# Optimization experiments

Hardware: AMD Instinct MI355X
Metric: run time of the kernel (lower is better)

## Reference

```python
import jax, jax.numpy as jnp
from jax import lax
import numpy as np
import math

D = 96   # d_model
H = 4    # num_heads (d_k = d_v = D per head, per the source)
K = 7    # depthwise kernel size
L = 4    # num conv layers


def _pos_encoding(seq_len, d):
    # Faithful to the source's (nonstandard) exponents: sin uses 2*i/d, cos uses 2*(i+1)/d
    pos = np.arange(seq_len, dtype=np.float32)[:, None]
    i = np.arange(0, d, 2, dtype=np.float32)
    pe = np.zeros((seq_len, d), dtype=np.float32)
    pe[:, 0::2] = np.sin(pos / 10000.0 ** (2.0 * i / d))
    pe[:, 1::2] = np.cos(pos / 10000.0 ** (2.0 * (i + 1.0) / d))
    return jnp.asarray(pe)


def _layernorm(x, g, b, eps=1e-5):
    m = jnp.mean(x, axis=-1, keepdims=True)
    v = jnp.mean((x - m) ** 2, axis=-1, keepdims=True)
    return (x - m) / jnp.sqrt(v + eps) * g + b


def setup_inputs() -> dict:
    key = jax.random.key(0)
    ks = jax.random.split(key, 10)
    B, S = 128, 384

    def xavier(k, shape, fan_in, fan_out):
        bound = math.sqrt(6.0 / (fan_in + fan_out))
        return jax.random.uniform(k, shape, jnp.float32, -bound, bound)

    return {
        "input": jax.random.normal(ks[0], (B, S, D), jnp.float32),
        "mask": jnp.zeros((B, S), dtype=bool),
        "conv_dw": jax.random.normal(ks[1], (L, D, 1, K), jnp.float32) * 0.05,
        "conv_dw_b": jnp.zeros((L, D), jnp.float32),
        "conv_pw": jax.random.normal(ks[2], (L, D, D, 1), jnp.float32) * 0.05,
        "conv_pw_b": jnp.zeros((L, D), jnp.float32),
        "WQ": xavier(ks[3], (H, D, D), D, D),
        "WK": xavier(ks[4], (H, D, D), D, D),
        "WV": xavier(ks[5], (H, D, D), D, D),
        "WO": xavier(ks[6], (H * D, D), H * D, D),
        "ffn_w1": jax.random.normal(ks[7], (D, D // 2), jnp.float32) * 0.1,
        "ffn_b1": jnp.zeros((D // 2,), jnp.float32),
        "ffn_w2": jax.random.normal(ks[8], (D // 2, D), jnp.float32) * 0.1,
        "ffn_b2": jnp.zeros((D,), jnp.float32),
        "ln_g": jnp.ones((L + 2, D), jnp.float32),
        "ln_b": jnp.zeros((L + 2, D), jnp.float32),
    }


def reference(input, mask, conv_dw, conv_dw_b, conv_pw, conv_pw_b,
              WQ, WK, WV, WO, ffn_w1, ffn_b1, ffn_w2, ffn_b2, ln_g, ln_b):
    B, S, _ = input.shape
    dn = ("NCH", "OIH", "NCH")

    # positional encoding (eval mode: all dropout is identity)
    x = input * jnp.float32(math.sqrt(D)) + _pos_encoding(S, D)[None]

    # conv blocks: LN -> depthwise conv -> pointwise conv -> relu -> residual
    for i in range(L):
        h = _layernorm(x, ln_g[i], ln_b[i])
        h = jnp.transpose(h, (0, 2, 1))  # [B, C, S]
        h = lax.conv_general_dilated(h, conv_dw[i], (1,), "SAME",
                                     feature_group_count=D, dimension_numbers=dn)
        h = h + conv_dw_b[i][None, :, None]
        h = lax.conv_general_dilated(h, conv_pw[i], (1,), "SAME", dimension_numbers=dn)
        h = jax.nn.relu(h + conv_pw_b[i][None, :, None])
        x = x + jnp.transpose(h, (0, 2, 1))

    # multi-head attention with per-head full-width projections (d_k = D)
    h = _layernorm(x, ln_g[L], ln_b[L])
    Q = jnp.einsum("bsd,hde->hbse", h, WQ)
    Kh = jnp.einsum("bsd,hde->hbse", h, WK)
    V = jnp.einsum("bsd,hde->hbse", h, WV)
    # source divides scores by temperature = 1/sqrt(d_k) => multiply by sqrt(D)
    scores = jnp.einsum("hbqe,hbke->hbqk", Q, Kh) * jnp.float32(math.sqrt(D))
    # mask is viewed [B, S, 1]: masks query rows, broadcast over keys
    scores = jnp.where(mask[None, :, :, None], -jnp.inf, scores)
    attn = jax.nn.softmax(scores, axis=-1)
    ctx = jnp.einsum("hbqk,hbke->hbqe", attn, V)
    cat = jnp.transpose(ctx, (1, 2, 0, 3)).reshape(B, S, H * D)
    x = x + cat @ WO

    # feed-forward: Linear -> sigmoid -> Linear, residual
    h2 = _layernorm(x, ln_g[L + 1], ln_b[L + 1])
    ff = jax.nn.sigmoid(h2 @ ffn_w1 + ffn_b1) @ ffn_w2 + ffn_b2
    return x + ff
```

## Files before the change

### kernel.cpp

```cpp
#include <hip/hip_runtime.h>
#include <math.h>


constexpr int B = 128;
constexpr int S = 384;
constexpr int D = 96;
constexpr int H = 4;
constexpr int KW = 7;
constexpr int L = 4;
constexpr int ROWS = B * S;
constexpr long long NTOT = (long long)ROWS * D;
constexpr float SQRTD = 9.797958971132712f;

typedef _Float16 f16x8 __attribute__((ext_vector_type(8)));
typedef float f32x4 __attribute__((ext_vector_type(4)));
typedef unsigned short us;
typedef unsigned short us8 __attribute__((ext_vector_type(8)));

__device__ __forceinline__ us f2h(float f) {
    _Float16 h = (_Float16)f;
    return __builtin_bit_cast(us, h);
}
__device__ __forceinline__ f16x8 ldh(const us* p) {
    return *reinterpret_cast<const f16x8*>(p);
}

__global__ void pe_kernel(float* __restrict__ pe) {
    int idx = blockIdx.x * 256 + threadIdx.x;
    if (idx >= S * D) return;
    int s = idx / D, c = idx - s * D;
    int j = c >> 1;
    float expo = (c & 1) ? (4.0f * j + 2.0f) / 96.0f : (4.0f * j) / 96.0f;
    float freq = expf(-expo * logf(10000.0f));
    float ang = (float)s * freq;
    pe[idx] = (c & 1) ? cosf(ang) : sinf(ang);
}

__global__ void prep_w(const float* __restrict__ WQ, const float* __restrict__ WK,
                       const float* __restrict__ cpw, const float* __restrict__ w1,
                       const float* __restrict__ w2,
                       us* __restrict__ wqS, us* __restrict__ wkS, us* __restrict__ pwS,
                       us* __restrict__ w1S, us* __restrict__ w2S) {
    int idx = blockIdx.x * 256 + threadIdx.x;
    if (idx >= H * D * D) return;
    int h = idx / (D * D), rem = idx - h * (D * D);
    int d = rem / D, e = rem - d * D;
    int n = e >> 4, lmod = e & 15, kk = d >> 5, ldiv = (d >> 3) & 3, j = d & 7;
    size_t fi = (size_t)(((n * 3 + kk) * 64 + ldiv * 16 + lmod) * 8 + j);
    wqS[(size_t)h * D * D + fi] = f2h(WQ[idx] * SQRTD);
    wkS[(size_t)h * D * D + fi] = f2h(WK[idx]);
    {
        int l = idx / (D * D);
        int o = rem / D, c = rem - o * D;
        int no = o >> 4, lo = o & 15, kc = c >> 5, lc = (c >> 3) & 3, jc = c & 7;
        pwS[(size_t)l * D * D + (size_t)(((no * 3 + kc) * 64 + lc * 16 + lo) * 8 + jc)] =
            f2h(cpw[idx]);
    }
    if (idx < 48 * 96) {
        int m = idx / 96, c = idx - m * 96;
        int nm = m >> 4, lm = m & 15, kc = c >> 5, lc = (c >> 3) & 3, jc = c & 7;
        w1S[((nm * 3 + kc) * 64 + lc * 16 + lm) * 8 + jc] = f2h(w1[c * 48 + m]);
    }
    if (idx < 96 * 64) {
        int o = idx / 64, mk = idx - o * 64;
        int no = o >> 4, lo = o & 15, km = mk >> 5, lm2 = (mk >> 3) & 3, jm = mk & 7;
        w2S[((no * 2 + km) * 64 + lm2 * 16 + lo) * 8 + jm] =
            (mk < 48) ? f2h(w2[mk * 96 + o]) : (us)0;
    }
}

__global__ void prep_wvo(const float* __restrict__ WV, const float* __restrict__ WO,
                         us* __restrict__ wvoS) {
    int blk = blockIdx.x;
    int h = blk / 6, ot = blk - h * 6;
    int tid = threadIdx.x;
    const float* wv = WV + (size_t)h * D * D;
    const float* wo = WO + (size_t)h * D * D;
    for (int i = tid; i < 16 * 96; i += 256) {
        int lmod = i / 96, d = i - (i / 96) * 96;
        int o = ot * 16 + lmod;
        float acc = 0.f;
        for (int e = 0; e < 96; e++) acc += wv[d * 96 + e] * wo[e * 96 + o];
        int kk = d >> 5, ldiv = (d >> 3) & 3, j = d & 7;
        wvoS[(size_t)h * D * D + (size_t)(((ot * 3 + kk) * 64 + ldiv * 16 + lmod) * 8 + j)] =
            f2h(acc);
    }
}

__global__ void conv0f(const float* __restrict__ in, const float* __restrict__ pe,
                       const float* __restrict__ g0, const float* __restrict__ b0,
                       float* __restrict__ xout, us* __restrict__ lnout,
                       const float* __restrict__ dwW, const float* __restrict__ dwB,
                       const us* __restrict__ pwW, const float* __restrict__ pwb,
                       const float* __restrict__ gnext, const float* __restrict__ bnext) {
    __shared__ us lnb_s[70 * 104];
    __shared__ us dwb_s[64 * 104];
    __shared__ float lw[96 * 8];
    int tid = threadIdx.x;
    int wave = tid >> 6, lane = tid & 63;
    int r0 = blockIdx.x * 64;
    int b = r0 / S, s0 = r0 % S;

    for (int i = tid; i < 96 * KW; i += 256) lw[(i / KW) * 8 + (i % KW)] = dwW[i];

    for (int i = wave; i < 70; i += 4) {
        int s = s0 - 3 + i;
        bool valid = (unsigned)s < (unsigned)S;
        float v0 = 0.f, v1 = 0.f;
        if (valid) {
            size_t ro = ((size_t)b * S + s) * 96;
            v0 = in[ro + lane] * SQRTD + pe[s * 96 + lane];
            v1 = (lane < 32) ? in[ro + 64 + lane] * SQRTD + pe[s * 96 + 64 + lane] : 0.f;
        }
        float sm = v0 + v1, q = v0 * v0 + v1 * v1;
        for (int off = 32; off > 0; off >>= 1) {
            sm += __shfl_xor(sm, off);
            q += __shfl_xor(q, off);
        }
        float mean = sm * (1.0f / D);
        float var = q * (1.0f / D) - mean * mean;
        float rstd = rsqrtf(var + 1e-5f);
        lnb_s[i * 104 + lane] = f2h(valid ? (v0 - mean) * rstd * g0[lane] + b0[lane] : 0.f);
        if (lane < 32)
            lnb_s[i * 104 + 64 + lane] =
                f2h(valid ? (v1 - mean) * rstd * g0[lane + 64] + b0[lane + 64] : 0.f);
    }
    __syncthreads();

    for (int u = tid; u < 768; u += 256) {
        int j = u / 12, c0 = (u - (u / 12) * 12) * 8;
        float acc[8];
        #pragma unroll
        for (int j2 = 0; j2 < 8; j2++) acc[j2] = dwB[c0 + j2];
        #pragma unroll
        for (int k = 0; k < KW; k++) {
            f16x8 v = ldh(&lnb_s[(j + k) * 104 + c0]);
            #pragma unroll
            for (int j2 = 0; j2 < 8; j2++) acc[j2] += (float)v[j2] * lw[(c0 + j2) * 8 + k];
        }
        us8 o;
        #pragma unroll
        for (int j2 = 0; j2 < 8; j2++) o[j2] = f2h(acc[j2]);
        *reinterpret_cast<us8*>(&dwb_s[j * 104 + c0]) = o;
    }
    __syncthreads();

    int lmod = lane & 15, ldiv = lane >> 4, m0 = wave * 16;
    f32x4 acc[6] = {};
    #pragma unroll
    for (int kk = 0; kk < 3; kk++) {
        f16x8 af = ldh(&dwb_s[(m0 + lmod) * 104 + kk * 32 + ldiv * 8]);
        #pragma unroll
        for (int n = 0; n < 6; n++) {
            f16x8 bf = ldh(pwW + (size_t)((n * 3 + kk) * 64) * 8 + lane * 8);
            acc[n] = __builtin_amdgcn_mfma_f32_16x16x32_f16(af, bf, acc[n], 0, 0, 0);
        }
    }

    float gv[6], bv2[6], pb[6];
    #pragma unroll
    for (int n = 0; n < 6; n++) {
        int o = n * 16 + lmod;
        gv[n] = gnext[o];
        bv2[n] = bnext[o];
        pb[n] = pwb[o];
    }
    #pragma unroll
    for (int n = 0; n < 6; n++) {
        int o = n * 16 + lmod;
        #pragma unroll
        for (int r = 0; r < 4; r++) {
            int sr = m0 + ldiv * 4 + r;
            size_t row = (size_t)r0 + sr;
            float base = in[row * 96 + o] * SQRTD + pe[(s0 + sr) * 96 + o];
            acc[n][r] = base + fmaxf(acc[n][r] + pb[n], 0.f);
        }
    }
    #pragma unroll
    for (int r = 0; r < 4; r++) {
        float sm = 0.f, qq = 0.f;
        #pragma unroll
        for (int n = 0; n < 6; n++) {
            sm += acc[n][r];
            qq += acc[n][r] * acc[n][r];
        }
        #pragma unroll
        for (int st = 1; st <= 8; st <<= 1) {
            sm += __shfl_xor(sm, st);
            qq += __shfl_xor(qq, st);
        }
        float mean = sm * (1.0f / D);
        float var = qq * (1.0f / D) - mean * mean;
        float rstd = rsqrtf(var + 1e-5f);
        size_t row = (size_t)r0 + m0 + ldiv * 4 + r;
        #pragma unroll
        for (int n = 0; n < 6; n++) {
            int o = n * 16 + lmod;
            xout[row * 96 + o] = acc[n][r];
            lnout[row * 96 + o] = f2h((acc[n][r] - mean) * rstd * gv[n] + bv2[n]);
        }
    }
}

__global__ void conv2(const float* __restrict__ xin, const us* __restrict__ lnin,
                      float* __restrict__ xout, us* __restrict__ lnout,
                      const float* __restrict__ dwW, const float* __restrict__ dwB,
                      const us* __restrict__ pwW, const float* __restrict__ pwb,
                      const float* __restrict__ gnext, const float* __restrict__ bnext) {
    __shared__ us dwb_s[64 * 104];
    __shared__ float lw[96 * 8];
    int tid = threadIdx.x;
    int wave = tid >> 6, lane = tid & 63;
    int r0 = blockIdx.x * 64;
    int b = r0 / S, s0 = r0 % S;

    for (int i = tid; i < 96 * KW; i += 256) lw[(i / KW) * 8 + (i % KW)] = dwW[i];
    __syncthreads();

    for (int u = tid; u < 768; u += 256) {
        int j = u / 12, c0 = (u - (u / 12) * 12) * 8;
        float acc[8];
        #pragma unroll
        for (int j2 = 0; j2 < 8; j2++) acc[j2] = dwB[c0 + j2];
        #pragma unroll
        for (int k = 0; k < KW; k++) {
            int ss = s0 + j + k - 3;
            if ((unsigned)ss < (unsigned)S) {
                f16x8 v = ldh(lnin + ((size_t)b * S + ss) * 96 + c0);
                #pragma unroll
                for (int j2 = 0; j2 < 8; j2++) acc[j2] += (float)v[j2] * lw[(c0 + j2) * 8 + k];
            }
        }
        us8 o;
        #pragma unroll
        for (int j2 = 0; j2 < 8; j2++) o[j2] = f2h(acc[j2]);
        *reinterpret_cast<us8*>(&dwb_s[j * 104 + c0]) = o;
    }
    __syncthreads();

    int lmod = lane & 15, ldiv = lane >> 4, m0 = wave * 16;
    f32x4 acc[6] = {};
    #pragma unroll
    for (int kk = 0; kk < 3; kk++) {
        f16x8 af = ldh(&dwb_s[(m0 + lmod) * 104 + kk * 32 + ldiv * 8]);
        #pragma unroll
        for (int n = 0; n < 6; n++) {
            f16x8 bf = ldh(pwW + (size_t)((n * 3 + kk) * 64) * 8 + lane * 8);
            acc[n] = __builtin_amdgcn_mfma_f32_16x16x32_f16(af, bf, acc[n], 0, 0, 0);
        }
    }

    float gv[6], bv2[6], pb[6];
    #pragma unroll
    for (int n = 0; n < 6; n++) {
        int o = n * 16 + lmod;
        gv[n] = gnext[o];
        bv2[n] = bnext[o];
        pb[n] = pwb[o];
    }
    #pragma unroll
    for (int n = 0; n < 6; n++) {
        #pragma unroll
        for (int r = 0; r < 4; r++) {
            size_t row = (size_t)r0 + m0 + ldiv * 4 + r;
            acc[n][r] = xin[row * 96 + n * 16 + lmod] + fmaxf(acc[n][r] + pb[n], 0.f);
        }
    }
    #pragma unroll
    for (int r = 0; r < 4; r++) {
        float sm = 0.f, qq = 0.f;
        #pragma unroll
        for (int n = 0; n < 6; n++) {
            sm += acc[n][r];
            qq += acc[n][r] * acc[n][r];
        }
        #pragma unroll
        for (int st = 1; st <= 8; st <<= 1) {
            sm += __shfl_xor(sm, st);
            qq += __shfl_xor(qq, st);
        }
        float mean = sm * (1.0f / D);
        float var = qq * (1.0f / D) - mean * mean;
        float rstd = rsqrtf(var + 1e-5f);
        size_t row = (size_t)r0 + m0 + ldiv * 4 + r;
        #pragma unroll
        for (int n = 0; n < 6; n++) {
            int o = n * 16 + lmod;
            xout[row * 96 + o] = acc[n][r];
            lnout[row * 96 + o] = f2h((acc[n][r] - mean) * rstd * gv[n] + bv2[n]);
        }
    }
}

__global__ void conv3p(const float* __restrict__ xin, const us* __restrict__ lnin,
                       float* __restrict__ xout, us* __restrict__ lnout,
                       const float* __restrict__ dwW, const float* __restrict__ dwB,
                       const us* __restrict__ pwW, const float* __restrict__ pwb,
                       const float* __restrict__ gnext, const float* __restrict__ bnext,
                       const us* __restrict__ wkS, const us* __restrict__ wvoS,
                       us* __restrict__ Kall, us* __restrict__ Vall) {
    __shared__ float lw[96 * 8];
    __shared__ us stg[96 * 72];
    __shared__ us lnstg[64 * 104];
    int tid = threadIdx.x;
    int wave = tid >> 6, lane = tid & 63;
    int lmod = lane & 15, ldiv = lane >> 4, m0 = wave * 16;
    int r0 = blockIdx.x * 64;
    int b = r0 / S, s0 = r0 % S;

    for (int i = tid; i < 96 * KW; i += 256) lw[(i / KW) * 8 + (i % KW)] = dwW[i];
    __syncthreads();

    for (int u = tid; u < 768; u += 256) {
        int j = u / 12, c0 = (u - (u / 12) * 12) * 8;
        float acc[8];
        #pragma unroll
        for (int j2 = 0; j2 < 8; j2++) acc[j2] = dwB[c0 + j2];
        #pragma unroll
        for (int k = 0; k < KW; k++) {
            int ss = s0 + j + k - 3;
            if ((unsigned)ss < (unsigned)S) {
                f16x8 v = ldh(lnin + ((size_t)b * S + ss) * 96 + c0);
                #pragma unroll
                for (int j2 = 0; j2 < 8; j2++) acc[j2] += (float)v[j2] * lw[(c0 + j2) * 8 + k];
            }
        }
        us8 o;
        #pragma unroll
        for (int j2 = 0; j2 < 8; j2++) o[j2] = f2h(acc[j2]);
        *reinterpret_cast<us8*>(&stg[j * 104 + c0]) = o;
    }
    __syncthreads();

    f32x4 acc[6] = {};
    #pragma unroll
    for (int kk = 0; kk < 3; kk++) {
        f16x8 af = ldh(&stg[(m0 + lmod) * 104 + kk * 32 + ldiv * 8]);
        #pragma unroll
        for (int n = 0; n < 6; n++) {
            f16x8 bf = ldh(pwW + (size_t)((n * 3 + kk) * 64) * 8 + lane * 8);
            acc[n] = __builtin_amdgcn_mfma_f32_16x16x32_f16(af, bf, acc[n], 0, 0, 0);
        }
    }

    float gv[6], bv2[6], pb[6];
    #pragma unroll
    for (int n = 0; n < 6; n++) {
        int o = n * 16 + lmod;
        gv[n] = gnext[o];
        bv2[n] = bnext[o];
        pb[n] = pwb[o];
    }
    #pragma unroll
    for (int n = 0; n < 6; n++) {
        #pragma unroll
        for (int r = 0; r < 4; r++) {
            size_t row = (size_t)r0 + m0 + ldiv * 4 + r;
            acc[n][r] = xin[row * 96 + n * 16 + lmod] + fmaxf(acc[n][r] + pb[n], 0.f);
        }
    }
    #pragma unroll
    for (int r = 0; r < 4; r++) {
        float sm = 0.f, qq = 0.f;
        #pragma unroll
        for (int n = 0; n < 6; n++) {
            sm += acc[n][r];
            qq += acc[n][r] * acc[n][r];
        }
        #pragma unroll
        for (int st = 1; st <= 8; st <<= 1) {
            sm += __shfl_xor(sm, st);
            qq += __shfl_xor(qq, st);
        }
        float mean = sm * (1.0f / D);
        float var = qq * (1.0f / D) - mean * mean;
        float rstd = rsqrtf(var + 1e-5f);
        size_t row = (size_t)r0 + m0 + ldiv * 4 + r;
        #pragma unroll
        for (int n = 0; n < 6; n++) {
            int o = n * 16 + lmod;
            xout[row * 96 + o] = acc[n][r];
            us hv = f2h((acc[n][r] - mean) * rstd * gv[n] + bv2[n]);
            lnout[row * 96 + o] = hv;
            lnstg[(m0 + ldiv * 4 + r) * 104 + o] = hv;
        }
    }
    __syncthreads();

    f16x8 af[3];
    #pragma unroll
    for (int kk = 0; kk < 3; kk++)
        af[kk] = ldh(&lnstg[(m0 + lmod) * 104 + kk * 32 + ldiv * 8]);

    for (int hd = 0; hd < H; hd++) {
        f32x4 ka[6] = {};
        #pragma unroll
        for (int kk = 0; kk < 3; kk++)
            #pragma unroll
            for (int n = 0; n < 6; n++) {
                f16x8 bf = ldh(wkS + (size_t)hd * D * D + (size_t)((n * 3 + kk) * 64) * 8 + lane * 8);
                ka[n] = __builtin_amdgcn_mfma_f32_16x16x32_f16(af[kk], bf, ka[n], 0, 0, 0);
            }
        __syncthreads();
        us* kT = stg + wave * 1664;
        #pragma unroll
        for (int n = 0; n < 6; n++)
            #pragma unroll
            for (int r = 0; r < 4; r++)
                kT[(ldiv * 4 + r) * 104 + n * 16 + lmod] = f2h(ka[n][r]);
        int t0 = (r0 % S) / 16 + wave;
        us* dst = Kall + (size_t)hd * NTOT + ((size_t)(b * 24 + t0) * 3) * 512;
        #pragma unroll
        for (int kk = 0; kk < 3; kk++) {
            us8 v = *reinterpret_cast<const us8*>(&kT[lmod * 104 + kk * 32 + ldiv * 8]);
            *reinterpret_cast<us8*>(dst + kk * 512 + lane * 8) = v;
        }
        f32x4 va[6] = {};
        #pragma unroll
        for (int kk = 0; kk < 3; kk++)
            #pragma unroll
            for (int n = 0; n < 6; n++) {
                f16x8 bf =
                    ldh(wvoS + (size_t)hd * D * D + (size_t)((n * 3 + kk) * 64) * 8 + lane * 8);
                va[n] = __builtin_amdgcn_mfma_f32_16x16x32_f16(af[kk], bf, va[n], 0, 0, 0);
            }
        __syncthreads();
        #pragma unroll
        for (int n = 0; n < 6; n++)
            #pragma unroll
            for (int r = 0; r < 4; r++)
                stg[(n * 16 + lmod) * 72 + m0 + ldiv * 4 + r] = f2h(va[n][r]);
        __syncthreads();
        int cblk = (r0 % S) / 64;
        us* dsth = Vall + (size_t)hd * NTOT;
        #pragma unroll
        for (int n = 0; n < 6; n++)
            #pragma unroll
            for (int kk = 0; kk < 2; kk++) {
                us8 v =
                    *reinterpret_cast<const us8*>(&stg[(n * 16 + lmod) * 72 + kk * 32 + ldiv * 8]);
                *reinterpret_cast<us8*>(
                    dsth + ((size_t)((b * 6 + cblk) * 6 + n) * 2 + kk) * 512 + lane * 8) = v;
            }
    }
}

__global__ __launch_bounds__(256, 2) void attn_g(const us* __restrict__ h16,
                                                 const us* __restrict__ wqS,
                                                 const us* __restrict__ Kall,
                                                 const us* __restrict__ Vall,
                                                 us* __restrict__ xpart) {
    __shared__ us Kb[2][6144];
    __shared__ us Vb[2][6144];
    __shared__ us Pq[4][3328];
    int tid = threadIdx.x, wave = tid >> 6, lane = tid & 63;
    int lmod = lane & 15, ldiv = lane >> 4;
    int p = blockIdx.x;
    int gl = (p & 7) * 192 + (p >> 3);
    int qt = gl % 3;
    int bh = gl / 3;
    int b = bh >> 2, hd = bh & 3;
    size_t rowbase = (size_t)b * S + qt * 128 + wave * 32;

    const us* Kh = Kall + (size_t)hd * NTOT + (size_t)b * 24 * 1536;
    const us* Vh = Vall + (size_t)hd * NTOT + (size_t)b * 36 * 1024;
    us* P = Pq[wave];

    us8 kst[3];
    #pragma unroll
    for (int j = 0; j < 3; j++)
        kst[j] = *reinterpret_cast<const us8*>(Kh + (size_t)(j * 256 + tid) * 8);

    f32x4 qa0[6] = {}, qa1[6] = {};
    #pragma unroll
    for (int kk = 0; kk < 3; kk++) {
        f16x8 a0 = ldh(h16 + (rowbase + lmod) * 96 + kk * 32 + ldiv * 8);
        f16x8 a1 = ldh(h16 + (rowbase + 16 + lmod) * 96 + kk * 32 + ldiv * 8);
        #pragma unroll
        for (int n = 0; n < 6; n++) {
            f16x8 bf = ldh(wqS + (size_t)hd * D * D + (size_t)((n * 3 + kk) * 64) * 8 + lane * 8);
            qa0[n] = __builtin_amdgcn_mfma_f32_16x16x32_f16(a0, bf, qa0[n], 0, 0, 0);
            qa1[n] = __builtin_amdgcn_mfma_f32_16x16x32_f16(a1, bf, qa1[n], 0, 0, 0);
        }
    }
    #pragma unroll
    for (int n = 0; n < 6; n++)
        #pragma unroll
        for (int r = 0; r < 4; r++) {
            P[(ldiv * 4 + r) * 104 + n * 16 + lmod] = f2h(qa0[n][r]);
            P[(16 + ldiv * 4 + r) * 104 + n * 16 + lmod] = f2h(qa1[n][r]);
        }
    f16x8 aq0[3], aq1[3];
    #pragma unroll
    for (int kk = 0; kk < 3; kk++) {
        aq0[kk] = ldh(&P[lmod * 104 + kk * 32 + ldiv * 8]);
        aq1[kk] = ldh(&P[(16 + lmod) * 104 + kk * 32 + ldiv * 8]);
    }
    #pragma unroll
    for (int j = 0; j < 3; j++)
        *reinterpret_cast<us8*>(&Kb[0][(j * 256 + tid) * 8]) = kst[j];
    __syncthreads();

    f32x4 mx0 = {-1e30f, -1e30f, -1e30f, -1e30f}, mx1 = mx0;
    for (int c = 0; c < 6; c++) {
        int cur = c & 1, nxt = cur ^ 1;
        us8 kn[3], vn[3];
        bool last = (c == 5);
        if (!last) {
            #pragma unroll
            for (int j = 0; j < 3; j++)
                kn[j] = *reinterpret_cast<const us8*>(Kh + (size_t)(c + 1) * 6144 +
                                                      (size_t)(j * 256 + tid) * 8);
        } else {
            #pragma unroll
            for (int j = 0; j < 3; j++) {
                kn[j] = *reinterpret_cast<const us8*>(Kh + (size_t)(j * 256 + tid) * 8);
                vn[j] = *reinterpret_cast<const us8*>(Vh + (size_t)(j * 256 + tid) * 8);
            }
        }
        __builtin_amdgcn_s_setprio(1);
        f32x4 s0[4] = {}, s1[4] = {};
        #pragma unroll
        for (int nt = 0; nt < 4; nt++)
            #pragma unroll
            for (int kk = 0; kk < 3; kk++) {
                f16x8 bf = ldh(&Kb[cur][(nt * 3 + kk) * 512 + lane * 8]);
                s0[nt] = __builtin_amdgcn_mfma_f32_16x16x32_f16(aq0[kk], bf, s0[nt], 0, 0, 0);
                s1[nt] = __builtin_amdgcn_mfma_f32_16x16x32_f16(aq1[kk], bf, s1[nt], 0, 0, 0);
            }
        __builtin_amdgcn_s_setprio(0);
        #pragma unroll
        for (int nt = 0; nt < 4; nt++)
            #pragma unroll
            for (int r = 0; r < 4; r++) {
                mx0[r] = fmaxf(mx0[r], s0[nt][r]);
                mx1[r] = fmaxf(mx1[r], s1[nt][r]);
            }
        int wb = last ? 0 : nxt;
        #pragma unroll
        for (int j = 0; j < 3; j++)
            *reinterpret_cast<us8*>(&Kb[wb][(j * 256 + tid) * 8]) = kn[j];
        if (last) {
            #pragma unroll
            for (int j = 0; j < 3; j++)
                *reinterpret_cast<us8*>(&Vb[0][(j * 256 + tid) * 8]) = vn[j];
        }
        __syncthreads();
    }
    #pragma unroll
    for (int st = 1; st <= 8; st <<= 1)
        #pragma unroll
        for (int r = 0; r < 4; r++) {
            mx0[r] = fmaxf(mx0[r], __shfl_xor(mx0[r], st));
            mx1[r] = fmaxf(mx1[r], __shfl_xor(mx1[r], st));
        }

    f32x4 oacc0[6] = {}, oacc1[6] = {};
    f32x4 l0v = {}, l1v = {};
    for (int c = 0; c < 6; c++) {
        int cur = c & 1, nxt = cur ^ 1;
        us8 kn[3], vn[3];
        if (c < 5) {
            #pragma unroll
            for (int j = 0; j < 3; j++) {
                kn[j] = *reinterpret_cast<const us8*>(Kh + (size_t)(c + 1) * 6144 +
                                                      (size_t)(j * 256 + tid) * 8);
                vn[j] = *reinterpret_cast<const us8*>(Vh + (size_t)(c + 1) * 6144 +
                                                      (size_t)(j * 256 + tid) * 8);
            }
        }
        __builtin_amdgcn_s_setprio(1);
        f32x4 s0[4] = {}, s1[4] = {};
        #pragma unroll
        for (int nt = 0; nt < 4; nt++)
            #pragma unroll
            for (int kk = 0; kk < 3; kk++) {
                f16x8 bf = ldh(&Kb[cur][(nt * 3 + kk) * 512 + lane * 8]);
                s0[nt] = __builtin_amdgcn_mfma_f32_16x16x32_f16(aq0[kk], bf, s0[nt], 0, 0, 0);
                s1[nt] = __builtin_amdgcn_mfma_f32_16x16x32_f16(aq1[kk], bf, s1[nt], 0, 0, 0);
            }
        __builtin_amdgcn_s_setprio(0);
        #pragma unroll
        for (int nt = 0; nt < 4; nt++)
            #pragma unroll
            for (int r = 0; r < 4; r++) {
                float p0 = __expf(s0[nt][r] - mx0[r]);
                float p1 = __expf(s1[nt][r] - mx1[r]);
                l0v[r] += p0;
                l1v[r] += p1;
                P[(ldiv * 4 + r) * 72 + nt * 16 + lmod] = f2h(p0);
                P[(16 + ldiv * 4 + r) * 72 + nt * 16 + lmod] = f2h(p1);
            }
        __builtin_amdgcn_s_setprio(1);
        #pragma unroll
        for (int kk = 0; kk < 2; kk++) {
            f16x8 pf0 = ldh(&P[lmod * 72 + kk * 32 + ldiv * 8]);
            f16x8 pf1 = ldh(&P[(16 + lmod) * 72 + kk * 32 + ldiv * 8]);
            #pragma unroll
            for (int n = 0; n < 6; n++) {
                f16x8 bf = ldh(&Vb[cur][(n * 2 + kk) * 512 + lane * 8]);
                oacc0[n] = __builtin_amdgcn_mfma_f32_16x16x32_f16(pf0, bf, oacc0[n], 0, 0, 0);
                oacc1[n] = __builtin_amdgcn_mfma_f32_16x16x32_f16(pf1, bf, oacc1[n], 0, 0, 0);
            }
        }
        __builtin_amdgcn_s_setprio(0);
        if (c < 5) {
            #pragma unroll
            for (int j = 0; j < 3; j++) {
                *reinterpret_cast<us8*>(&Kb[nxt][(j * 256 + tid) * 8]) = kn[j];
                *reinterpret_cast<us8*>(&Vb[nxt][(j * 256 + tid) * 8]) = vn[j];
            }
            __syncthreads();
        }
    }
    #pragma unroll
    for (int st = 1; st <= 8; st <<= 1)
        #pragma unroll
        for (int r = 0; r < 4; r++) {
            l0v[r] += __shfl_xor(l0v[r], st);
            l1v[r] += __shfl_xor(l1v[r], st);
        }

    us* xp = xpart + (size_t)hd * NTOT;
    #pragma unroll
    for (int r = 0; r < 4; r++) {
        float inv0 = 1.f / l0v[r];
        float inv1 = 1.f / l1v[r];
        #pragma unroll
        for (int n = 0; n < 6; n++) {
            xp[(rowbase + ldiv * 4 + r) * 96 + n * 16 + lmod] = f2h(oacc0[n][r] * inv0);
            xp[(rowbase + 16 + ldiv * 4 + r) * 96 + n * 16 + lmod] = f2h(oacc1[n][r] * inv1);
        }
    }
}

__global__ void ffn_ln(const float* __restrict__ x, const us* __restrict__ xpart,
                       const float* __restrict__ gln, const float* __restrict__ bln,
                       const us* __restrict__ w1S, const float* __restrict__ b1,
                       const us* __restrict__ w2S, const float* __restrict__ b2,
                       float* __restrict__ out) {
    __shared__ float xf[64 * 96];
    __shared__ us lnb[64 * 104];
    __shared__ us mid[64 * 72];
    int tid = threadIdx.x, wave = tid >> 6, lane = tid & 63;
    int lmod = lane & 15, ldiv = lane >> 4, m0 = wave * 16;
    int row0 = blockIdx.x * 64;

    for (int i = wave; i < 64; i += 4) {
        size_t ro = (size_t)(row0 + i) * 96;
        float v0 = x[ro + lane];
        float v1 = (lane < 32) ? x[ro + 64 + lane] : 0.f;
        #pragma unroll
        for (int h = 0; h < H; h++) {
            const us* xp = xpart + (size_t)h * NTOT + ro;
            v0 += (float)__builtin_bit_cast(_Float16, xp[lane]);
            if (lane < 32) v1 += (float)__builtin_bit_cast(_Float16, xp[64 + lane]);
        }
        xf[i * 96 + lane] = v0;
        if (lane < 32) xf[i * 96 + 64 + lane] = v1;
        float sm = v0 + v1, q = v0 * v0 + v1 * v1;
        for (int off = 32; off > 0; off >>= 1) {
            sm += __shfl_xor(sm, off);
            q += __shfl_xor(q, off);
        }
        float mean = sm * (1.0f / D);
        float var = q * (1.0f / D) - mean * mean;
        float rstd = rsqrtf(var + 1e-5f);
        lnb[i * 104 + lane] = f2h((v0 - mean) * rstd * gln[lane] + bln[lane]);
        if (lane < 32)
            lnb[i * 104 + 64 + lane] = f2h((v1 - mean) * rstd * gln[lane + 64] + bln[lane + 64]);
    }
    __syncthreads();

    f32x4 a3[3] = {};
    #pragma unroll
    for (int kk = 0; kk < 3; kk++) {
        f16x8 af = ldh(&lnb[(m0 + lmod) * 104 + kk * 32 + ldiv * 8]);
        #pragma unroll
        for (int n = 0; n < 3; n++) {
            f16x8 bf = ldh(w1S + (size_t)((n * 3 + kk) * 64) * 8 + lane * 8);
            a3[n] = __builtin_amdgcn_mfma_f32_16x16x32_f16(af, bf, a3[n], 0, 0, 0);
        }
    }
    #pragma unroll
    for (int n = 0; n < 3; n++) {
        float bv = b1[n * 16 + lmod];
        #pragma unroll
        for (int r = 0; r < 4; r++) {
            float v = a3[n][r] + bv;
            mid[(m0 + ldiv * 4 + r) * 72 + n * 16 + lmod] = f2h(1.f / (1.f + __expf(-v)));
        }
    }
    #pragma unroll
    for (int r = 0; r < 4; r++) mid[(m0 + ldiv * 4 + r) * 72 + 48 + lmod] = 0;
    __syncthreads();

    f32x4 a6[6] = {};
    #pragma unroll
    for (int kk = 0; kk < 2; kk++) {
        f16x8 af = ldh(&mid[(m0 + lmod) * 72 + kk * 32 + ldiv * 8]);
        #pragma unroll
        for (int n = 0; n < 6; n++) {
            f16x8 bf = ldh(w2S + (size_t)((n * 2 + kk) * 64) * 8 + lane * 8);
            a6[n] = __builtin_amdgcn_mfma_f32_16x16x32_f16(af, bf, a6[n], 0, 0, 0);
        }
    }
    #pragma unroll
    for (int n = 0; n < 6; n++) {
        int o = n * 16 + lmod;
        float bv = b2[o];
        #pragma unroll
        for (int r = 0; r < 4; r++) {
            int sr = m0 + ldiv * 4 + r;
            out[(size_t)(row0 + sr) * 96 + o] = xf[sr * 96 + o] + a6[n][r] + bv;
        }
    }
}

extern "C" void kernel_launch(void* const* d_in, const int* in_sizes, int n_in,
                              void* d_out, int out_size, void* d_ws, size_t ws_size,
                              hipStream_t stream) {
    const float* in   = (const float*)d_in[0];
    const float* cdw  = (const float*)d_in[2];
    const float* cdwb = (const float*)d_in[3];
    const float* cpw  = (const float*)d_in[4];
    const float* cpwb = (const float*)d_in[5];
    const float* WQ   = (const float*)d_in[6];
    const float* WK   = (const float*)d_in[7];
    const float* WV   = (const float*)d_in[8];
    const float* WO   = (const float*)d_in[9];
    const float* w1   = (const float*)d_in[10];
    const float* b1   = (const float*)d_in[11];
    const float* w2   = (const float*)d_in[12];
    const float* b2   = (const float*)d_in[13];
    const float* lng  = (const float*)d_in[14];
    const float* lnb  = (const float*)d_in[15];
    float* out = (float*)d_out;
    float* ws = (float*)d_ws;

    float* xA  = ws;
    float* xB  = xA + NTOT;
    float* pe  = xB + NTOT;
    us* lnA    = (us*)(pe + S * D);
    us* lnB    = lnA + NTOT;
    us* Kall   = lnB + NTOT;
    us* Vall   = Kall + (size_t)H * NTOT;
    us* xpart  = Vall + (size_t)H * NTOT;
    us* wqS    = xpart + (size_t)H * NTOT;
    us* wkS    = wqS + H * D * D;
    us* wvoS   = wkS + H * D * D;
    us* pwS    = wvoS + H * D * D;
    us* w1S    = pwS + L * D * D;
    us* w2S    = w1S + 48 * 96;

    pe_kernel<<<(S * D + 255) / 256, 256, 0, stream>>>(pe);
    prep_w<<<(H * D * D + 255) / 256, 256, 0, stream>>>(WQ, WK, cpw, w1, w2,
                                                        wqS, wkS, pwS, w1S, w2S);
    prep_wvo<<<H * 6, 256, 0, stream>>>(WV, WO, wvoS);

    conv0f<<<ROWS / 64, 256, 0, stream>>>(in, pe, lng, lnb, xA, lnB,
                                          cdw, cdwb, pwS, cpwb, lng + D, lnb + D);
    conv2<<<ROWS / 64, 256, 0, stream>>>(xA, lnB, xB, lnA, cdw + D * KW, cdwb + D,
                                         pwS + D * D, cpwb + D, lng + 2 * D, lnb + 2 * D);
    conv2<<<ROWS / 64, 256, 0, stream>>>(xB, lnA, xA, lnB, cdw + 2 * D * KW, cdwb + 2 * D,
                                         pwS + 2 * D * D, cpwb + 2 * D, lng + 3 * D,
                                         lnb + 3 * D);
    conv3p<<<ROWS / 64, 256, 0, stream>>>(xA, lnB, xB, lnA, cdw + 3 * D * KW, cdwb + 3 * D,
                                          pwS + 3 * D * D, cpwb + 3 * D, lng + 4 * D,
                                          lnb + 4 * D, wkS, wvoS, Kall, Vall);

    attn_g<<<1536, 256, 0, stream>>>(lnA, wqS, Kall, Vall, xpart);

    ffn_ln<<<ROWS / 64, 256, 0, stream>>>(xB, xpart, lng + 5 * D, lnb + 5 * D,
                                          w1S, b1, w2S, b2, out);
}
```

Before: 280.1 us.

## Halve attention key chunk size and pool LDS to cut shared-memory footprint

The attention kernel now streams K/V in 32-key chunks instead of 64, reorders the V layout written by the projection kernel to match, and overlays the Q staging area with the K/V buffers in one pooled shared array. The aim is to shrink LDS use (about 34 KB versus roughly 75 KB) so more workgroups can be resident per CU, improving latency hiding. In exchange the kernel runs twice as many loop iterations, each with fewer MFMAs and its own barrier, and adds an extra sync before K is first stored.

```diff
diff --git a/kernel.cpp b/kernel.cpp
--- a/kernel.cpp
+++ b/kernel.cpp
@@ -440,7 +440,7 @@
                 us8 v =
                     *reinterpret_cast<const us8*>(&stg[(n * 16 + lmod) * 72 + kk * 32 + ldiv * 8]);
                 *reinterpret_cast<us8*>(
-                    dsth + ((size_t)((b * 6 + cblk) * 6 + n) * 2 + kk) * 512 + lane * 8) = v;
+                    dsth + ((size_t)((b * 12 + cblk * 2 + kk) * 6 + n)) * 512 + lane * 8) = v;
             }
     }
 }
@@ -450,9 +450,7 @@
                                                  const us* __restrict__ Kall,
                                                  const us* __restrict__ Vall,
                                                  us* __restrict__ xpart) {
-    __shared__ us Kb[2][6144];
-    __shared__ us Vb[2][6144];
-    __shared__ us Pq[4][3328];
+    __shared__ us pool[17408];
     int tid = threadIdx.x, wave = tid >> 6, lane = tid & 63;
     int lmod = lane & 15, ldiv = lane >> 4;
     int p = blockIdx.x;
@@ -464,12 +462,12 @@
 
     const us* Kh = Kall + (size_t)hd * NTOT + (size_t)b * 24 * 1536;
     const us* Vh = Vall + (size_t)hd * NTOT + (size_t)b * 36 * 1024;
-    us* P = Pq[wave];
-
-    us8 kst[3];
-    #pragma unroll
-    for (int j = 0; j < 3; j++)
-        kst[j] = *reinterpret_cast<const us8*>(Kh + (size_t)(j * 256 + tid) * 8);
+    us* P = pool + 12288 + wave * 1280;
+    bool has1 = tid < 128;
+
+    us8 k00, k01;
+    k00 = *reinterpret_cast<const us8*>(Kh + (size_t)tid * 8);
+    if (has1) k01 = *reinterpret_cast<const us8*>(Kh + (size_t)(256 + tid) * 8);
 
     f32x4 qa0[6] = {}, qa1[6] = {};
     #pragma unroll
@@ -483,67 +481,64 @@
             qa1[n] = __builtin_amdgcn_mfma_f32_16x16x32_f16(a1, bf, qa1[n], 0, 0, 0);
         }
     }
+    us* qst = pool + wave * 3328;
     #pragma unroll
     for (int n = 0; n < 6; n++)
         #pragma unroll
         for (int r = 0; r < 4; r++) {
-            P[(ldiv * 4 + r) * 104 + n * 16 + lmod] = f2h(qa0[n][r]);
-            P[(16 + ldiv * 4 + r) * 104 + n * 16 + lmod] = f2h(qa1[n][r]);
+            qst[(ldiv * 4 + r) * 104 + n * 16 + lmod] = f2h(qa0[n][r]);
+            qst[(16 + ldiv * 4 + r) * 104 + n * 16 + lmod] = f2h(qa1[n][r]);
         }
     f16x8 aq0[3], aq1[3];
     #pragma unroll
     for (int kk = 0; kk < 3; kk++) {
-        aq0[kk] = ldh(&P[lmod * 104 + kk * 32 + ldiv * 8]);
-        aq1[kk] = ldh(&P[(16 + lmod) * 104 + kk * 32 + ldiv * 8]);
-    }
-    #pragma unroll
-    for (int j = 0; j < 3; j++)
-        *reinterpret_cast<us8*>(&Kb[0][(j * 256 + tid) * 8]) = kst[j];
+        aq0[kk] = ldh(&qst[lmod * 104 + kk * 32 + ldiv * 8]);
+        aq1[kk] = ldh(&qst[(16 + lmod) * 104 + kk * 32 + ldiv * 8]);
+    }
+    __syncthreads();
+    *reinterpret_cast<us8*>(&pool[tid * 8]) = k00;
+    if (has1) *reinterpret_cast<us8*>(&pool[(256 + tid) * 8]) = k01;
     __syncthreads();
 
     f32x4 mx0 = {-1e30f, -1e30f, -1e30f, -1e30f}, mx1 = mx0;
-    for (int c = 0; c < 6; c++) {
-        int cur = c & 1, nxt = cur ^ 1;
-        us8 kn[3], vn[3];
-        bool last = (c == 5);
+    for (int c = 0; c < 12; c++) {
+        us* kbc = pool + (c & 1) * 3072;
+        us8 kn0, kn1, vn0, vn1;
+        bool last = (c == 11);
         if (!last) {
-            #pragma unroll
-            for (int j = 0; j < 3; j++)
-                kn[j] = *reinterpret_cast<const us8*>(Kh + (size_t)(c + 1) * 6144 +
-                                                      (size_t)(j * 256 + tid) * 8);
+            const us* src = Kh + (size_t)(c + 1) * 3072;
+            kn0 = *reinterpret_cast<const us8*>(src + (size_t)tid * 8);
+            if (has1) kn1 = *reinterpret_cast<const us8*>(src + (size_t)(256 + tid) * 8);
         } else {
-            #pragma unroll
-            for (int j = 0; j < 3; j++) {
-                kn[j] = *reinterpret_cast<const us8*>(Kh + (size_t)(j * 256 + tid) * 8);
-                vn[j] = *reinterpret_cast<const us8*>(Vh + (size_t)(j * 256 + tid) * 8);
-            }
+            kn0 = *reinterpret_cast<const us8*>(Kh + (size_t)tid * 8);
+            if (has1) kn1 = *reinterpret_cast<const us8*>(Kh + (size_t)(256 + tid) * 8);
+            vn0 = *reinterpret_cast<const us8*>(Vh + (size_t)tid * 8);
+            if (has1) vn1 = *reinterpret_cast<const us8*>(Vh + (size_t)(256 + tid) * 8);
         }
         __builtin_amdgcn_s_setprio(1);
-        f32x4 s0[4] = {}, s1[4] = {};
-        #pragma unroll
-        for (int nt = 0; nt < 4; nt++)
+        f32x4 s0[2] = {}, s1[2] = {};
+        #pragma unroll
+        for (int nt = 0; nt < 2; nt++)
             #pragma unroll
             for (int kk = 0; kk < 3; kk++) {
-                f16x8 bf = ldh(&Kb[cur][(nt * 3 + kk) * 512 + lane * 8]);
+                f16x8 bf = ldh(&kbc[(nt * 3 + kk) * 512 + lane * 8]);
                 s0[nt] = __builtin_amdgcn_mfma_f32_16x16x32_f16(aq0[kk], bf, s0[nt], 0, 0, 0);
                 s1[nt] = __builtin_amdgcn_mfma_f32_16x16x32_f16(aq1[kk], bf, s1[nt], 0, 0, 0);
             }
         __builtin_amdgcn_s_setprio(0);
         #pragma unroll
-        for (int nt = 0; nt < 4; nt++)
+        for (int nt = 0; nt < 2; nt++)
             #pragma unroll
             for (int r = 0; r < 4; r++) {
                 mx0[r] = fmaxf(mx0[r], s0[nt][r]);
                 mx1[r] = fmaxf(mx1[r], s1[nt][r]);
             }
-        int wb = last ? 0 : nxt;
-        #pragma unroll
-        for (int j = 0; j < 3; j++)
-            *reinterpret_cast<us8*>(&Kb[wb][(j * 256 + tid) * 8]) = kn[j];
+        us* kbw = pool + (last ? 0 : ((c & 1) ^ 1)) * 3072;
+        *reinterpret_cast<us8*>(&kbw[tid * 8]) = kn0;
+        if (has1) *reinterpret_cast<us8*>(&kbw[(256 + tid) * 8]) = kn1;
         if (last) {
-            #pragma unroll
-            for (int j = 0; j < 3; j++)
-                *reinterpret_cast<us8*>(&Vb[0][(j * 256 + tid) * 8]) = vn[j];
+            *reinterpret_cast<us8*>(&pool[6144 + tid * 8]) = vn0;
+            if (has1) *reinterpret_cast<us8*>(&pool[6144 + (256 + tid) * 8]) = vn1;
         }
         __syncthreads();
     }
@@ -557,58 +552,62 @@
 
     f32x4 oacc0[6] = {}, oacc1[6] = {};
     f32x4 l0v = {}, l1v = {};
-    for (int c = 0; c < 6; c++) {
-        int cur = c & 1, nxt = cur ^ 1;
-        us8 kn[3], vn[3];
-        if (c < 5) {
-            #pragma unroll
-            for (int j = 0; j < 3; j++) {
-                kn[j] = *reinterpret_cast<const us8*>(Kh + (size_t)(c + 1) * 6144 +
-                                                      (size_t)(j * 256 + tid) * 8);
-                vn[j] = *reinterpret_cast<const us8*>(Vh + (size_t)(c + 1) * 6144 +
-                                                      (size_t)(j * 256 + tid) * 8);
+    for (int c = 0; c < 12; c++) {
+        us* kbc = pool + (c & 1) * 3072;
+        us* vbc = pool + 6144 + (c & 1) * 3072;
+        us8 kn0, kn1, vn0, vn1;
+        if (c < 11) {
+            const us* ksrc = Kh + (size_t)(c + 1) * 3072;
+            const us* vsrc = Vh + (size_t)(c + 1) * 3072;
+            kn0 = *reinterpret_cast<const us8*>(ksrc + (size_t)tid * 8);
+            vn0 = *reinterpret_cast<const us8*>(vsrc + (size_t)tid * 8);
+            if (has1) {
+                kn1 = *reinterpret_cast<const us8*>(ksrc + (size_t)(256 + tid) * 8);
+                vn1 = *reinterpret_cast<const us8*>(vsrc + (size_t)(256 + tid) * 8);
             }
         }
         __builtin_amdgcn_s_setprio(1);
-        f32x4 s0[4] = {}, s1[4] = {};
-        #pragma unroll
-        for (int nt = 0; nt < 4; nt++)
+        f32x4 s0[2] = {}, s1[2] = {};
+        #pragma unroll
+        for (int nt = 0; nt < 2; nt++)
             #pragma unroll
             for (int kk = 0; kk < 3; kk++) {
-                f16x8 bf = ldh(&Kb[cur][(nt * 3 + kk) * 512 + lane * 8]);
+                f16x8 bf = ldh(&kbc[(nt * 3 + kk) * 512 + lane * 8]);
                 s0[nt] = __builtin_amdgcn_mfma_f32_16x16x32_f16(aq0[kk], bf, s0[nt], 0, 0, 0);
                 s1[nt] = __builtin_amdgcn_mfma_f32_16x16x32_f16(aq1[kk], bf, s1[nt], 0, 0, 0);
             }
         __builtin_amdgcn_s_setprio(0);
         #pragma unroll
-        for (int nt = 0; nt < 4; nt++)
+        for (int nt = 0; nt < 2; nt++)
             #pragma unroll
             for (int r = 0; r < 4; r++) {
                 float p0 = __expf(s0[nt][r] - mx0[r]);
                 float p1 = __expf(s1[nt][r] - mx1[r]);
                 l0v[r] += p0;
                 l1v[r] += p1;
-                P[(ldiv * 4 + r) * 72 + nt * 16 + lmod] = f2h(p0);
-                P[(16 + ldiv * 4 + r) * 72 + nt * 16 + lmod] = f2h(p1);
+                P[(ldiv * 4 + r) * 40 + nt * 16 + lmod] = f2h(p0);
+                P[(16 + ldiv * 4 + r) * 40 + nt * 16 + lmod] = f2h(p1);
             }
         __builtin_amdgcn_s_setprio(1);
-        #pragma unroll
-        for (int kk = 0; kk < 2; kk++) {
-            f16x8 pf0 = ldh(&P[lmod * 72 + kk * 32 + ldiv * 8]);
-            f16x8 pf1 = ldh(&P[(16 + lmod) * 72 + kk * 32 + ldiv * 8]);
+        {
+            f16x8 pf0 = ldh(&P[lmod * 40 + ldiv * 8]);
+            f16x8 pf1 = ldh(&P[(16 + lmod) * 40 + ldiv * 8]);
             #pragma unroll
             for (int n = 0; n < 6; n++) {
-                f16x8 bf = ldh(&Vb[cur][(n * 2 + kk) * 512 + lane * 8]);
+                f16x8 bf = ldh(&vbc[n * 512 + lane * 8]);
                 oacc0[n] = __builtin_amdgcn_mfma_f32_16x16x32_f16(pf0, bf, oacc0[n], 0, 0, 0);
                 oacc1[n] = __builtin_amdgcn_mfma_f32_16x16x32_f16(pf1, bf, oacc1[n], 0, 0, 0);
             }
         }
         __builtin_amdgcn_s_setprio(0);
-        if (c < 5) {
-            #pragma unroll
-            for (int j = 0; j < 3; j++) {
-                *reinterpret_cast<us8*>(&Kb[nxt][(j * 256 + tid) * 8]) = kn[j];
-                *reinterpret_cast<us8*>(&Vb[nxt][(j * 256 + tid) * 8]) = vn[j];
+        if (c < 11) {
+            us* kbn = pool + ((c & 1) ^ 1) * 3072;
+            us* vbn = pool + 6144 + ((c & 1) ^ 1) * 3072;
+            *reinterpret_cast<us8*>(&kbn[tid * 8]) = kn0;
+            *reinterpret_cast<us8*>(&vbn[tid * 8]) = vn0;
+            if (has1) {
+                *reinterpret_cast<us8*>(&kbn[(256 + tid) * 8]) = kn1;
+                *reinterpret_cast<us8*>(&vbn[(256 + tid) * 8]) = vn1;
             }
             __syncthreads();
         }
```

Measured after the change: 284.8 us. No clear change (+1.7%).

## Enlarge attention query tile to 48 rows per wave and alias shared memory

Applied to the files above, without the earlier changes.

Each wave now handles 48 query rows instead of 32, so a block covers 192 queries and the grid drops from 1536 to 1024 blocks. Each K/V chunk loaded into shared memory is reused across more query rows, which cuts global K/V traffic and synchronisation per query. Shared buffers are merged into one pool, with the Q staging area aliased over the K/V buffers and an extra barrier added. The cost is higher register pressure from a third set of accumulators, which may hurt occupancy under launch_bounds(256,2), and fewer blocks to spread across CUs.

```diff
diff --git a/kernel.cpp b/kernel.cpp
--- a/kernel.cpp
+++ b/kernel.cpp
@@ -450,67 +450,71 @@
                                                  const us* __restrict__ Kall,
                                                  const us* __restrict__ Vall,
                                                  us* __restrict__ xpart) {
-    __shared__ us Kb[2][6144];
-    __shared__ us Vb[2][6144];
-    __shared__ us Pq[4][3328];
+    __shared__ us pool[38400];
     int tid = threadIdx.x, wave = tid >> 6, lane = tid & 63;
     int lmod = lane & 15, ldiv = lane >> 4;
     int p = blockIdx.x;
-    int gl = (p & 7) * 192 + (p >> 3);
-    int qt = gl % 3;
-    int bh = gl / 3;
+    int gl = (p & 7) * 128 + (p >> 3);
+    int qt = gl & 1;
+    int bh = gl >> 1;
     int b = bh >> 2, hd = bh & 3;
-    size_t rowbase = (size_t)b * S + qt * 128 + wave * 32;
+    size_t rowbase = (size_t)b * S + qt * 192 + wave * 48;
 
     const us* Kh = Kall + (size_t)hd * NTOT + (size_t)b * 24 * 1536;
     const us* Vh = Vall + (size_t)hd * NTOT + (size_t)b * 36 * 1024;
-    us* P = Pq[wave];
-
-    us8 kst[3];
+    us* P = pool + 24576 + wave * 3456;
+
+    us8 k0s[3];
     #pragma unroll
     for (int j = 0; j < 3; j++)
-        kst[j] = *reinterpret_cast<const us8*>(Kh + (size_t)(j * 256 + tid) * 8);
-
-    f32x4 qa0[6] = {}, qa1[6] = {};
+        k0s[j] = *reinterpret_cast<const us8*>(Kh + (size_t)(j * 256 + tid) * 8);
+
+    f32x4 qa0[6] = {}, qa1[6] = {}, qa2[6] = {};
     #pragma unroll
     for (int kk = 0; kk < 3; kk++) {
         f16x8 a0 = ldh(h16 + (rowbase + lmod) * 96 + kk * 32 + ldiv * 8);
         f16x8 a1 = ldh(h16 + (rowbase + 16 + lmod) * 96 + kk * 32 + ldiv * 8);
+        f16x8 a2 = ldh(h16 + (rowbase + 32 + lmod) * 96 + kk * 32 + ldiv * 8);
         #pragma unroll
         for (int n = 0; n < 6; n++) {
             f16x8 bf = ldh(wqS + (size_t)hd * D * D + (size_t)((n * 3 + kk) * 64) * 8 + lane * 8);
             qa0[n] = __builtin_amdgcn_mfma_f32_16x16x32_f16(a0, bf, qa0[n], 0, 0, 0);
             qa1[n] = __builtin_amdgcn_mfma_f32_16x16x32_f16(a1, bf, qa1[n], 0, 0, 0);
-        }
-    }
+            qa2[n] = __builtin_amdgcn_mfma_f32_16x16x32_f16(a2, bf, qa2[n], 0, 0, 0);
+        }
+    }
+    us* qst = pool + wave * 4992;
     #pragma unroll
     for (int n = 0; n < 6; n++)
         #pragma unroll
         for (int r = 0; r < 4; r++) {
-            P[(ldiv * 4 + r) * 104 + n * 16 + lmod] = f2h(qa0[n][r]);
-            P[(16 + ldiv * 4 + r) * 104 + n * 16 + lmod] = f2h(qa1[n][r]);
-        }
-    f16x8 aq0[3], aq1[3];
+            qst[(ldiv * 4 + r) * 104 + n * 16 + lmod] = f2h(qa0[n][r]);
+            qst[(16 + ldiv * 4 + r) * 104 + n * 16 + lmod] = f2h(qa1[n][r]);
+            qst[(32 + ldiv * 4 + r) * 104 + n * 16 + lmod] = f2h(qa2[n][r]);
+        }
+    f16x8 aq0[3], aq1[3], aq2[3];
     #pragma unroll
     for (int kk = 0; kk < 3; kk++) {
-        aq0[kk] = ldh(&P[lmod * 104 + kk * 32 + ldiv * 8]);
-        aq1[kk] = ldh(&P[(16 + lmod) * 104 + kk * 32 + ldiv * 8]);
-    }
+        aq0[kk] = ldh(&qst[lmod * 104 + kk * 32 + ldiv * 8]);
+        aq1[kk] = ldh(&qst[(16 + lmod) * 104 + kk * 32 + ldiv * 8]);
+        aq2[kk] = ldh(&qst[(32 + lmod) * 104 + kk * 32 + ldiv * 8]);
+    }
+    __syncthreads();
     #pragma unroll
     for (int j = 0; j < 3; j++)
-        *reinterpret_cast<us8*>(&Kb[0][(j * 256 + tid) * 8]) = kst[j];
-    __syncthreads();
-
-    f32x4 mx0 = {-1e30f, -1e30f, -1e30f, -1e30f}, mx1 = mx0;
+        *reinterpret_cast<us8*>(&pool[(j * 256 + tid) * 8]) = k0s[j];
+    __syncthreads();
+
+    f32x4 mx0 = {-1e30f, -1e30f, -1e30f, -1e30f}, mx1 = mx0, mx2 = mx0;
     for (int c = 0; c < 6; c++) {
-        int cur = c & 1, nxt = cur ^ 1;
+        us* kbc = pool + (c & 1) * 6144;
         us8 kn[3], vn[3];
         bool last = (c == 5);
         if (!last) {
+            const us* src = Kh + (size_t)(c + 1) * 6144;
             #pragma unroll
             for (int j = 0; j < 3; j++)
-                kn[j] = *reinterpret_cast<const us8*>(Kh + (size_t)(c + 1) * 6144 +
-                                                      (size_t)(j * 256 + tid) * 8);
+                kn[j] = *reinterpret_cast<const us8*>(src + (size_t)(j * 256 + tid) * 8);
         } else {
             #pragma unroll
             for (int j = 0; j < 3; j++) {
@@ -519,14 +523,15 @@
             }
         }
         __builtin_amdgcn_s_setprio(1);
-        f32x4 s0[4] = {}, s1[4] = {};
+        f32x4 s0[4] = {}, s1[4] = {}, s2[4] = {};
         #pragma unroll
         for (int nt = 0; nt < 4; nt++)
             #pragma unroll
             for (int kk = 0; kk < 3; kk++) {
-                f16x8 bf = ldh(&Kb[cur][(nt * 3 + kk) * 512 + lane * 8]);
+                f16x8 bf = ldh(&kbc[(nt * 3 + kk) * 512 + lane * 8]);
                 s0[nt] = __builtin_amdgcn_mfma_f32_16x16x32_f16(aq0[kk], bf, s0[nt], 0, 0, 0);
                 s1[nt] = __builtin_amdgcn_mfma_f32_16x16x32_f16(aq1[kk], bf, s1[nt], 0, 0, 0);
+                s2[nt] = __builtin_amdgcn_mfma_f32_16x16x32_f16(aq2[kk], bf, s2[nt], 0, 0, 0);
             }
         __builtin_amdgcn_s_setprio(0);
         #pragma unroll
@@ -535,15 +540,16 @@
             for (int r = 0; r < 4; r++) {
                 mx0[r] = fmaxf(mx0[r], s0[nt][r]);
                 mx1[r] = fmaxf(mx1[r], s1[nt][r]);
-            }
-        int wb = last ? 0 : nxt;
+                mx2[r] = fmaxf(mx2[r], s2[nt][r]);
+            }
+        us* kbw = pool + (last ? 0 : ((c & 1) ^ 1)) * 6144;
         #pragma unroll
         for (int j = 0; j < 3; j++)
-            *reinterpret_cast<us8*>(&Kb[wb][(j * 256 + tid) * 8]) = kn[j];
+            *reinterpret_cast<us8*>(&kbw[(j * 256 + tid) * 8]) = kn[j];
         if (last) {
             #pragma unroll
             for (int j = 0; j < 3; j++)
-                *reinterpret_cast<us8*>(&Vb[0][(j * 256 + tid) * 8]) = vn[j];
+                *reinterpret_cast<us8*>(&pool[12288 + (j * 256 + tid) * 8]) = vn[j];
         }
         __syncthreads();
     }
@@ -553,31 +559,34 @@
         for (int r = 0; r < 4; r++) {
             mx0[r] = fmaxf(mx0[r], __shfl_xor(mx0[r], st));
             mx1[r] = fmaxf(mx1[r], __shfl_xor(mx1[r], st));
-        }
-
-    f32x4 oacc0[6] = {}, oacc1[6] = {};
-    f32x4 l0v = {}, l1v = {};
+            mx2[r] = fmaxf(mx2[r], __shfl_xor(mx2[r], st));
+        }
+
+    f32x4 oacc0[6] = {}, oacc1[6] = {}, oacc2[6] = {};
+    f32x4 l0v = {}, l1v = {}, l2v = {};
     for (int c = 0; c < 6; c++) {
-        int cur = c & 1, nxt = cur ^ 1;
+        us* kbc = pool + (c & 1) * 6144;
+        us* vbc = pool + 12288 + (c & 1) * 6144;
         us8 kn[3], vn[3];
         if (c < 5) {
+            const us* ksrc = Kh + (size_t)(c + 1) * 6144;
+            const us* vsrc = Vh + (size_t)(c + 1) * 6144;
             #pragma unroll
             for (int j = 0; j < 3; j++) {
-                kn[j] = *reinterpret_cast<const us8*>(Kh + (size_t)(c + 1) * 6144 +
-                                                      (size_t)(j * 256 + tid) * 8);
-                vn[j] = *reinterpret_cast<const us8*>(Vh + (size_t)(c + 1) * 6144 +
-                                                      (size_t)(j * 256 + tid) * 8);
+                kn[j] = *reinterpret_cast<const us8*>(ksrc + (size_t)(j * 256 + tid) * 8);
+                vn[j] = *reinterpret_cast<const us8*>(vsrc + (size_t)(j * 256 + tid) * 8);
             }
         }
         __builtin_amdgcn_s_setprio(1);
-        f32x4 s0[4] = {}, s1[4] = {};
+        f32x4 s0[4] = {}, s1[4] = {}, s2[4] = {};
         #pragma unroll
         for (int nt = 0; nt < 4; nt++)
             #pragma unroll
             for (int kk = 0; kk < 3; kk++) {
-                f16x8 bf = ldh(&Kb[cur][(nt * 3 + kk) * 512 + lane * 8]);
+                f16x8 bf = ldh(&kbc[(nt * 3 + kk) * 512 + lane * 8]);
                 s0[nt] = __builtin_amdgcn_mfma_f32_16x16x32_f16(aq0[kk], bf, s0[nt], 0, 0, 0);
                 s1[nt] = __builtin_amdgcn_mfma_f32_16x16x32_f16(aq1[kk], bf, s1[nt], 0, 0, 0);
+                s2[nt] = __builtin_amdgcn_mfma_f32_16x16x32_f16(aq2[kk], bf, s2[nt], 0, 0, 0);
             }
         __builtin_amdgcn_s_setprio(0);
         #pragma unroll
@@ -586,29 +595,36 @@
             for (int r = 0; r < 4; r++) {
                 float p0 = __expf(s0[nt][r] - mx0[r]);
                 float p1 = __expf(s1[nt][r] - mx1[r]);
+                float p2 = __expf(s2[nt][r] - mx2[r]);
                 l0v[r] += p0;
                 l1v[r] += p1;
+                l2v[r] += p2;
                 P[(ldiv * 4 + r) * 72 + nt * 16 + lmod] = f2h(p0);
                 P[(16 + ldiv * 4 + r) * 72 + nt * 16 + lmod] = f2h(p1);
+                P[(32 + ldiv * 4 + r) * 72 + nt * 16 + lmod] = f2h(p2);
             }
         __builtin_amdgcn_s_setprio(1);
         #pragma unroll
         for (int kk = 0; kk < 2; kk++) {
             f16x8 pf0 = ldh(&P[lmod * 72 + kk * 32 + ldiv * 8]);
             f16x8 pf1 = ldh(&P[(16 + lmod) * 72 + kk * 32 + ldiv * 8]);
+            f16x8 pf2 = ldh(&P[(32 + lmod) * 72 + kk * 32 + ldiv * 8]);
             #pragma unroll
             for (int n = 0; n < 6; n++) {
-                f16x8 bf = ldh(&Vb[cur][(n * 2 + kk) * 512 + lane * 8]);
+                f16x8 bf = ldh(&vbc[(n * 2 + kk) * 512 + lane * 8]);
                 oacc0[n] = __builtin_amdgcn_mfma_f32_16x16x32_f16(pf0, bf, oacc0[n], 0, 0, 0);
                 oacc1[n] = __builtin_amdgcn_mfma_f32_16x16x32_f16(pf1, bf, oacc1[n], 0, 0, 0);
+                oacc2[n] = __builtin_amdgcn_mfma_f32_16x16x32_f16(pf2, bf, oacc2[n], 0, 0, 0);
             }
         }
         __builtin_amdgcn_s_setprio(0);
         if (c < 5) {
+            us* kbn = pool + ((c & 1) ^ 1) * 6144;
+            us* vbn = pool + 12288 + ((c & 1) ^ 1) * 6144;
             #pragma unroll
             for (int j = 0; j < 3; j++) {
-                *reinterpret_cast<us8*>(&Kb[nxt][(j * 256 + tid) * 8]) = kn[j];
-                *reinterpret_cast<us8*>(&Vb[nxt][(j * 256 + tid) * 8]) = vn[j];
+                *reinterpret_cast<us8*>(&kbn[(j * 256 + tid) * 8]) = kn[j];
+                *reinterpret_cast<us8*>(&vbn[(j * 256 + tid) * 8]) = vn[j];
             }
             __syncthreads();
         }
@@ -619,6 +635,7 @@
         for (int r = 0; r < 4; r++) {
             l0v[r] += __shfl_xor(l0v[r], st);
             l1v[r] += __shfl_xor(l1v[r], st);
+            l2v[r] += __shfl_xor(l2v[r], st);
         }
 
     us* xp = xpart + (size_t)hd * NTOT;
@@ -626,10 +643,12 @@
     for (int r = 0; r < 4; r++) {
         float inv0 = 1.f / l0v[r];
         float inv1 = 1.f / l1v[r];
+        float inv2 = 1.f / l2v[r];
         #pragma unroll
         for (int n = 0; n < 6; n++) {
             xp[(rowbase + ldiv * 4 + r) * 96 + n * 16 + lmod] = f2h(oacc0[n][r] * inv0);
             xp[(rowbase + 16 + ldiv * 4 + r) * 96 + n * 16 + lmod] = f2h(oacc1[n][r] * inv1);
+            xp[(rowbase + 32 + ldiv * 4 + r) * 96 + n * 16 + lmod] = f2h(oacc2[n][r] * inv2);
         }
     }
 }
@@ -769,7 +788,7 @@
                                           pwS + 3 * D * D, cpwb + 3 * D, lng + 4 * D,
                                           lnb + 4 * D, wkS, wvoS, Kall, Vall);
 
-    attn_g<<<1536, 256, 0, stream>>>(lnA, wqS, Kall, Vall, xpart);
+    attn_g<<<1024, 256, 0, stream>>>(lnA, wqS, Kall, Vall, xpart);
 
     ffn_ln<<<ROWS / 64, 256, 0, stream>>>(xB, xpart, lng + 5 * D, lnb + 5 * D,
                                           w1S, b1, w2S, b2, out);
```

New measurement: 275.5 us. About the same (-1.6%).
